# Kernel tuning notes

Hardware: AMD Instinct MI355X
Metric: run time of the kernel (lower is better)

The kernel has to match this reference:

```python
import jax, jax.numpy as jnp
import numpy as np

N = 65536   # nodes
E = 524288  # edges (avg degree 8)
IN, H, Z = 256, 128, 32
LN_EPS = 1e-5


def setup_inputs() -> dict:
    key = jax.random.key(0)
    ks = jax.random.split(key, 6)
    x = jax.random.normal(ks[0], (N, IN), jnp.float32)
    edge_index = jax.random.randint(ks[1], (2, E), 0, N, jnp.int32)
    W1 = jax.random.normal(ks[2], (IN, H), jnp.float32) / np.sqrt(IN)
    W2 = jax.random.normal(ks[3], (H, H), jnp.float32) / np.sqrt(H)
    W3 = jax.random.normal(ks[4], (H, Z), jnp.float32) / np.sqrt(H)
    return dict(
        x=x, edge_index=edge_index,
        ln_w=jnp.ones((IN,), jnp.float32), ln_b=jnp.zeros((IN,), jnp.float32),
        W1=W1, b1=jnp.zeros((H,), jnp.float32),
        W2=W2, b2=jnp.zeros((H,), jnp.float32),
        W3=W3, b3=jnp.zeros((Z,), jnp.float32),
    )


def _layer_norm(x, w, b):
    mu = jnp.mean(x, axis=-1, keepdims=True)
    var = jnp.mean(jnp.square(x - mu), axis=-1, keepdims=True)
    return (x - mu) * jax.lax.rsqrt(var + LN_EPS) * w + b


def _gcn_conv(x, W, b, src, dst, n):
    # PyG GCNConv: transform, add self-loops, symmetric deg normalization, scatter-add.
    x = x @ W  # [N, out]
    ones = jnp.ones(src.shape[0], x.dtype)
    deg = jax.ops.segment_sum(ones, dst, num_segments=n) + 1.0  # +1 self-loop
    dis = jax.lax.rsqrt(deg)  # deg^{-1/2}
    norm = dis[src] * dis[dst]  # [E]
    agg = jax.ops.segment_sum(x[src] * norm[:, None], dst, num_segments=n)
    agg = agg + x * (dis * dis)[:, None]  # self-loop term: dis[i]*dis[i]
    return agg + b


def reference(x, edge_index, ln_w, ln_b, W1, b1, W2, b2, W3, b3):
    src, dst = edge_index[0], edge_index[1]
    n = x.shape[0]
    h = _layer_norm(x, ln_w, ln_b)
    h = jax.nn.relu(_gcn_conv(h, W1, b1, src, dst, n))
    # dropout is identity in eval mode
    h = jax.nn.relu(_gcn_conv(h, W2, b2, src, dst, n))
    return _gcn_conv(h, W3, b3, src, dst, n)
```

## Files before the change

kernel.cpp:

```cpp
#include <hip/hip_runtime.h>
#include <hip/hip_bf16.h>

#define FIN 256
#define FH 128
#define FZ 32

typedef unsigned short u16;
typedef unsigned int u32;
typedef __attribute__((ext_vector_type(4))) float f32x4;
typedef __attribute__((ext_vector_type(8))) _Float16 f16x8;
typedef __attribute__((ext_vector_type(4))) _Float16 f16x4;
typedef __attribute__((ext_vector_type(4))) unsigned int uint4v;

__device__ inline u16 f2h(float v) { return __builtin_bit_cast(u16, (_Float16)v); }

__global__ __launch_bounds__(256) void prep(const float* __restrict__ W1,
                                            const float* __restrict__ W2,
                                            const float* __restrict__ W3,
                                            u16* __restrict__ w1h, u16* __restrict__ w2h,
                                            u16* __restrict__ w3h, int* __restrict__ deg,
                                            int* __restrict__ total) {
    int b = blockIdx.x, t = threadIdx.x;
    if (b < 256) {
        deg[b * 256 + t] = 0;
        if (b == 0 && t == 0) *total = 0;
        return;
    }
    int i = (b - 256) * 256 + t;
    if (i < FIN * FH) {
        int k = i / FH, n = i % FH;
        w1h[n * FIN + k] = f2h(W1[i]);
    } else if (i < FIN * FH + FH * FH) {
        int j = i - FIN * FH;
        int k = j / FH, n = j % FH;
        w2h[n * FH + k] = f2h(W2[j]);
    } else {
        int j = i - (FIN * FH + FH * FH);
        int k = j / FZ, n = j % FZ;
        w3h[n * FH + k] = f2h(W3[j]);
    }
}

__global__ void deg_count(const int* __restrict__ dst, int* __restrict__ deg,
                          int* __restrict__ erank, int E) {
    int e = blockIdx.x * 256 + threadIdx.x;
    if (e < E) erank[e] = atomicAdd(&deg[dst[e]], 1);
}

__global__ __launch_bounds__(256) void scan_fused(const int* __restrict__ deg,
                                                  int* __restrict__ total,
                                                  int* __restrict__ rowstart,
                                                  float* __restrict__ dis) {
    __shared__ int s[256];
    __shared__ int base;
    int t = threadIdx.x;
    int i = blockIdx.x * 256 + t;
    int v = deg[i];
    s[t] = v;
    __syncthreads();
    for (int o = 1; o < 256; o <<= 1) {
        int add = (t >= o) ? s[t - o] : 0;
        __syncthreads();
        s[t] += add;
        __syncthreads();
    }
    if (t == 255) base = atomicAdd(total, s[255]);
    __syncthreads();
    rowstart[i] = s[t] - v + base;
    dis[i] = rsqrtf((float)v + 1.0f);
}

__global__ __launch_bounds__(512) void gemm_ln(
    const float* __restrict__ Xf, const u16* __restrict__ Wg,
    const float* __restrict__ lnw, const float* __restrict__ lnb,
    const float* __restrict__ dis, u16* __restrict__ Y,
    const int* __restrict__ src, const int* __restrict__ dst,
    const int* __restrict__ erank, const int* __restrict__ rowstart,
    int* __restrict__ csrc, int E) {
    constexpr int K = FIN, N = FH;
    constexpr int BM = 128, NT = N / 16, NK = K / 32;

    __shared__ u16 Wl[N * K];

    const int t = threadIdx.x;
    const int row0 = blockIdx.x * BM;
    const int wave = t >> 6, l = t & 63;
    const int lm = l & 15, lq = l >> 4;
    const int row = row0 + wave * 16 + lm;

    const float* xr = Xf + (long long)row * K;
    f16x8 a[NK];
    float s = 0.f, ss = 0.f;
#pragma unroll
    for (int kk = 0; kk < NK; ++kk) {
        f32x4 x0 = *(const f32x4*)(xr + kk * 32 + lq * 8);
        f32x4 x1 = *(const f32x4*)(xr + kk * 32 + lq * 8 + 4);
#pragma unroll
        for (int c = 0; c < 4; ++c) {
            s += x0[c] + x1[c];
            ss += x0[c] * x0[c] + x1[c] * x1[c];
            a[kk][c] = (_Float16)x0[c];
            a[kk][4 + c] = (_Float16)x1[c];
        }
    }
    s += __shfl_xor(s, 16);
    ss += __shfl_xor(ss, 16);
    s += __shfl_xor(s, 32);
    ss += __shfl_xor(ss, 32);
    float mu = s * (1.0f / K);
    float rs = rsqrtf(fmaxf(ss * (1.0f / K) - mu * mu, 0.f) + 1e-5f);

    for (int i = t; i < N * K / 8; i += 512) {
        int nn = i / (K / 8), k8 = i % (K / 8);
        *(uint4v*)&Wl[nn * K + ((k8 ^ (nn & 7)) * 8)] = *(const uint4v*)&Wg[nn * K + k8 * 8];
    }

#pragma unroll
    for (int kk = 0; kk < NK; ++kk) {
        f32x4 w0 = *(const f32x4*)(lnw + kk * 32 + lq * 8);
        f32x4 w1 = *(const f32x4*)(lnw + kk * 32 + lq * 8 + 4);
        f32x4 c0 = *(const f32x4*)(lnb + kk * 32 + lq * 8);
        f32x4 c1 = *(const f32x4*)(lnb + kk * 32 + lq * 8 + 4);
#pragma unroll
        for (int c = 0; c < 4; ++c) {
            a[kk][c] = (_Float16)(((float)a[kk][c] - mu) * rs * w0[c] + c0[c]);
            a[kk][4 + c] = (_Float16)(((float)a[kk][4 + c] - mu) * rs * w1[c] + c1[c]);
        }
    }
    __syncthreads();

    f32x4 acc[NT];
#pragma unroll
    for (int i = 0; i < NT; ++i) acc[i] = (f32x4){0.f, 0.f, 0.f, 0.f};
#pragma unroll
    for (int kk = 0; kk < NK; ++kk) {
#pragma unroll
        for (int nt = 0; nt < NT; ++nt) {
            int nn = nt * 16 + lm;
            f16x8 wv = *(const f16x8*)&Wl[nn * K + (((kk * 4 + lq) ^ (nn & 7)) * 8)];
            acc[nt] = __builtin_amdgcn_mfma_f32_16x16x32_f16(wv, a[kk], acc[nt], 0, 0, 0);
        }
    }

    const float di = dis[row];
    u16* yr = Y + (long long)row * N;
#pragma unroll
    for (int nt = 0; nt < NT; ++nt) {
        f16x4 v;
#pragma unroll
        for (int r = 0; r < 4; ++r) v[r] = (_Float16)(acc[nt][r] * di);
        *(f16x4*)&yr[nt * 16 + lq * 4] = v;
    }

    {
        int epb = E / gridDim.x;
        int base = blockIdx.x * epb;
        for (int j = t; j < epb; j += 512) {
            int e = base + j;
            int d = dst[e];
            csrc[rowstart[d] + erank[e]] = src[e];
        }
    }
}

template <int K, int N>
__global__ __launch_bounds__(512) void gather_gemm(
    const u16* __restrict__ T, const u16* __restrict__ Wg,
    const int* __restrict__ rowstart, const int* __restrict__ degv,
    const int* __restrict__ csrc, const float* __restrict__ dis,
    const float* __restrict__ bias, u16* __restrict__ Y) {
    constexpr int BM = 128, NT = N / 16, NK = K / 32;

    __shared__ u16 Wl[N * K];
    __shared__ float bl[K];

    const int t = threadIdx.x;
    const int row0 = blockIdx.x * BM;
    const int wave = t >> 6, l = t & 63;
    const int lm = l & 15, lq = l >> 4;
    const int row = row0 + wave * 16 + lm;

    for (int i = t; i < N * K / 8; i += 512) {
        int nn = i / (K / 8), k8 = i % (K / 8);
        *(uint4v*)&Wl[nn * K + ((k8 ^ (nn & 7)) * 8)] = *(const uint4v*)&Wg[nn * K + k8 * 8];
    }
    if (t < K / 4) *(f32x4*)&bl[t * 4] = *(const f32x4*)&bias[t * 4];

    const float di = dis[row];
    const int rs = rowstart[row], dg = degv[row];
    float g[NK][8];
    {
        const u16* tr = T + (long long)row * K;
#pragma unroll
        for (int kk = 0; kk < NK; ++kk) {
            f16x8 v = *(const f16x8*)&tr[kk * 32 + lq * 8];
#pragma unroll
            for (int j = 0; j < 8; ++j) g[kk][j] = (float)v[j];
        }
    }
    int e = rs, e1 = rs + dg;
    for (; e + 1 < e1; e += 2) {
        int s0 = csrc[e], s1 = csrc[e + 1];
        const u16* t0 = T + (long long)s0 * K;
        const u16* t1 = T + (long long)s1 * K;
#pragma unroll
        for (int kk = 0; kk < NK; ++kk) {
            f16x8 v0 = *(const f16x8*)&t0[kk * 32 + lq * 8];
            f16x8 v1 = *(const f16x8*)&t1[kk * 32 + lq * 8];
#pragma unroll
            for (int j = 0; j < 8; ++j) g[kk][j] += (float)v0[j] + (float)v1[j];
        }
    }
    if (e < e1) {
        const u16* t0 = T + (long long)csrc[e] * K;
#pragma unroll
        for (int kk = 0; kk < NK; ++kk) {
            f16x8 v0 = *(const f16x8*)&t0[kk * 32 + lq * 8];
#pragma unroll
            for (int j = 0; j < 8; ++j) g[kk][j] += (float)v0[j];
        }
    }
    __syncthreads();

    f16x8 a[NK];
#pragma unroll
    for (int kk = 0; kk < NK; ++kk) {
#pragma unroll
        for (int j = 0; j < 8; ++j) {
            float h = fmaxf(g[kk][j] * di + bl[kk * 32 + lq * 8 + j], 0.f);
            a[kk][j] = (_Float16)h;
        }
    }

    f32x4 acc[NT];
#pragma unroll
    for (int i = 0; i < NT; ++i) acc[i] = (f32x4){0.f, 0.f, 0.f, 0.f};
#pragma unroll
    for (int kk = 0; kk < NK; ++kk) {
#pragma unroll
        for (int nt = 0; nt < NT; ++nt) {
            int nn = nt * 16 + lm;
            f16x8 wv = *(const f16x8*)&Wl[nn * K + (((kk * 4 + lq) ^ (nn & 7)) * 8)];
            acc[nt] = __builtin_amdgcn_mfma_f32_16x16x32_f16(wv, a[kk], acc[nt], 0, 0, 0);
        }
    }

    u16* yr = Y + (long long)row * N;
#pragma unroll
    for (int nt = 0; nt < NT; ++nt) {
        f16x4 v;
#pragma unroll
        for (int r = 0; r < 4; ++r) v[r] = (_Float16)(acc[nt][r] * di);
        *(f16x4*)&yr[nt * 16 + lq * 4] = v;
    }
}

__global__ __launch_bounds__(256) void agg32h(
    const u16* __restrict__ T, const int* __restrict__ rowstart, const int* __restrict__ degv,
    const int* __restrict__ csrc, const float* __restrict__ dis, const float* __restrict__ bias,
    float* __restrict__ OUT) {
    int node = blockIdx.x * 4 + (threadIdx.x >> 6);
    int l = threadIdx.x & 63;
    int h = l >> 3, c = l & 7;
    float di = dis[node];
    f32x4 acc = (f32x4){0.f, 0.f, 0.f, 0.f};
    if (h == 0) {
        f16x4 s = *(const f16x4*)&T[(long long)node * 32 + c * 4];
#pragma unroll
        for (int i = 0; i < 4; ++i) acc[i] = (float)s[i];
    }
    int e0 = rowstart[node];
    int e1 = e0 + degv[node];
    int e = e0 + h;
    for (; e + 8 < e1; e += 16) {
        int s0 = csrc[e], s1 = csrc[e + 8];
        f16x4 u0 = *(const f16x4*)&T[(long long)s0 * 32 + c * 4];
        f16x4 u1 = *(const f16x4*)&T[(long long)s1 * 32 + c * 4];
#pragma unroll
        for (int i = 0; i < 4; ++i) acc[i] += (float)u0[i] + (float)u1[i];
    }
    if (e < e1) {
        int s0 = csrc[e];
        f16x4 u0 = *(const f16x4*)&T[(long long)s0 * 32 + c * 4];
#pragma unroll
        for (int i = 0; i < 4; ++i) acc[i] += (float)u0[i];
    }
#pragma unroll
    for (int m = 8; m <= 32; m <<= 1) {
#pragma unroll
        for (int i = 0; i < 4; ++i) acc[i] += __shfl_xor(acc[i], m);
    }
    if (h == 0) {
        f32x4 b0 = *(const f32x4*)(bias + c * 4);
        f32x4 r;
#pragma unroll
        for (int i = 0; i < 4; ++i) r[i] = acc[i] * di + b0[i];
        *(f32x4*)(OUT + (long long)node * 32 + c * 4) = r;
    }
}

extern "C" void kernel_launch(void* const* d_in, const int* in_sizes, int n_in,
                              void* d_out, int out_size, void* d_ws, size_t ws_size,
                              hipStream_t stream) {
    const float* x = (const float*)d_in[0];
    const int* ei = (const int*)d_in[1];
    const float* lnw = (const float*)d_in[2];
    const float* lnb = (const float*)d_in[3];
    const float* W1 = (const float*)d_in[4];
    const float* b1 = (const float*)d_in[5];
    const float* W2 = (const float*)d_in[6];
    const float* b2 = (const float*)d_in[7];
    const float* W3 = (const float*)d_in[8];
    const float* b3 = (const float*)d_in[9];
    float* out = (float*)d_out;

    const int n = in_sizes[0] / FIN;
    const int E = in_sizes[1] / 2;
    const int* src = ei;
    const int* dst = ei + E;

    char* w = (char*)d_ws;
    auto alloc = [&](size_t bytes) {
        char* p = w;
        w += (bytes + 255) & ~(size_t)255;
        return p;
    };
    int* deg = (int*)alloc((size_t)n * 4);
    int* rowstart = (int*)alloc((size_t)n * 4);
    int* erank = (int*)alloc((size_t)E * 4);
    int* total = (int*)alloc(256);
    float* dis = (float*)alloc((size_t)n * 4);
    int* csrc = (int*)alloc((size_t)E * 4);
    u16* w1h = (u16*)alloc(FIN * FH * 2);
    u16* w2h = (u16*)alloc(FH * FH * 2);
    u16* w3h = (u16*)alloc(FH * FZ * 2);
    u16* bufA = (u16*)alloc((size_t)n * FH * 2);
    u16* bufB = (u16*)alloc((size_t)n * FH * 2);

    prep<<<464, 256, 0, stream>>>(W1, W2, W3, w1h, w2h, w3h, deg, total);
    deg_count<<<E / 256, 256, 0, stream>>>(dst, deg, erank, E);
    scan_fused<<<n / 256, 256, 0, stream>>>(deg, total, rowstart, dis);
    gemm_ln<<<n / 128, 512, 0, stream>>>(x, w1h, lnw, lnb, dis, bufA,
                                         src, dst, erank, rowstart, csrc, E);
    gather_gemm<FH, FH><<<n / 128, 512, 0, stream>>>(bufA, w2h, rowstart, deg, csrc, dis, b1, bufB);
    gather_gemm<FH, FZ><<<n / 128, 512, 0, stream>>>(bufB, w3h, rowstart, deg, csrc, dis, b2, bufA);
    agg32h<<<n / 4, 256, 0, stream>>>(bufA, rowstart, deg, csrc, dis, b3, out);
}
```

Measured before the change: 145.1 us.

## Fuse weight prep with degree count, double rows per gemm_ln block, unroll gather

```diff
diff --git a/kernel.cpp b/kernel.cpp
--- a/kernel.cpp
+++ b/kernel.cpp
@@ -14,19 +14,17 @@
 
 __device__ inline u16 f2h(float v) { return __builtin_bit_cast(u16, (_Float16)v); }
 
-__global__ __launch_bounds__(256) void prep(const float* __restrict__ W1,
-                                            const float* __restrict__ W2,
-                                            const float* __restrict__ W3,
-                                            u16* __restrict__ w1h, u16* __restrict__ w2h,
-                                            u16* __restrict__ w3h, int* __restrict__ deg,
-                                            int* __restrict__ total) {
+__global__ __launch_bounds__(256) void prep_deg(
+    const float* __restrict__ W1, const float* __restrict__ W2, const float* __restrict__ W3,
+    u16* __restrict__ w1h, u16* __restrict__ w2h, u16* __restrict__ w3h,
+    const int* __restrict__ dst, int* __restrict__ deg, int* __restrict__ erank, int E) {
     int b = blockIdx.x, t = threadIdx.x;
-    if (b < 256) {
-        deg[b * 256 + t] = 0;
-        if (b == 0 && t == 0) *total = 0;
+    if (b >= 208) {
+        int e = (b - 208) * 256 + t;
+        if (e < E) erank[e] = atomicAdd(&deg[dst[e]], 1);
         return;
     }
-    int i = (b - 256) * 256 + t;
+    int i = b * 256 + t;
     if (i < FIN * FH) {
         int k = i / FH, n = i % FH;
         w1h[n * FIN + k] = f2h(W1[i]);
@@ -39,12 +37,6 @@
         int k = j / FZ, n = j % FZ;
         w3h[n * FH + k] = f2h(W3[j]);
     }
-}
-
-__global__ void deg_count(const int* __restrict__ dst, int* __restrict__ deg,
-                          int* __restrict__ erank, int E) {
-    int e = blockIdx.x * 256 + threadIdx.x;
-    if (e < E) erank[e] = atomicAdd(&deg[dst[e]], 1);
 }
 
 __global__ __launch_bounds__(256) void scan_fused(const int* __restrict__ deg,
@@ -70,7 +62,7 @@
     dis[i] = rsqrtf((float)v + 1.0f);
 }
 
-__global__ __launch_bounds__(512) void gemm_ln(
+__global__ __launch_bounds__(512, 4) void gemm_ln(
     const float* __restrict__ Xf, const u16* __restrict__ Wg,
     const float* __restrict__ lnw, const float* __restrict__ lnb,
     const float* __restrict__ dis, u16* __restrict__ Y,
@@ -78,43 +70,43 @@
     const int* __restrict__ erank, const int* __restrict__ rowstart,
     int* __restrict__ csrc, int E) {
     constexpr int K = FIN, N = FH;
-    constexpr int BM = 128, NT = N / 16, NK = K / 32;
+    constexpr int NT = N / 16, NK = K / 32;
 
     __shared__ u16 Wl[N * K];
 
     const int t = threadIdx.x;
-    const int row0 = blockIdx.x * BM;
     const int wave = t >> 6, l = t & 63;
     const int lm = l & 15, lq = l >> 4;
-    const int row = row0 + wave * 16 + lm;
-
-    const float* xr = Xf + (long long)row * K;
-    f16x8 a[NK];
-    float s = 0.f, ss = 0.f;
-#pragma unroll
-    for (int kk = 0; kk < NK; ++kk) {
-        f32x4 x0 = *(const f32x4*)(xr + kk * 32 + lq * 8);
-        f32x4 x1 = *(const f32x4*)(xr + kk * 32 + lq * 8 + 4);
+    const int row0 = blockIdx.x * 256 + wave * 16 + lm;
+    const int row1 = row0 + 128;
+
+    const float* xr0 = Xf + (long long)row0 * K;
+    f16x8 a0[NK];
+    float s0 = 0.f, ss0 = 0.f;
+#pragma unroll
+    for (int kk = 0; kk < NK; ++kk) {
+        f32x4 x0 = *(const f32x4*)(xr0 + kk * 32 + lq * 8);
+        f32x4 x1 = *(const f32x4*)(xr0 + kk * 32 + lq * 8 + 4);
 #pragma unroll
         for (int c = 0; c < 4; ++c) {
-            s += x0[c] + x1[c];
-            ss += x0[c] * x0[c] + x1[c] * x1[c];
-            a[kk][c] = (_Float16)x0[c];
-            a[kk][4 + c] = (_Float16)x1[c];
-        }
-    }
-    s += __shfl_xor(s, 16);
-    ss += __shfl_xor(ss, 16);
-    s += __shfl_xor(s, 32);
-    ss += __shfl_xor(ss, 32);
-    float mu = s * (1.0f / K);
-    float rs = rsqrtf(fmaxf(ss * (1.0f / K) - mu * mu, 0.f) + 1e-5f);
+            s0 += x0[c] + x1[c];
+            ss0 += x0[c] * x0[c] + x1[c] * x1[c];
+            a0[kk][c] = (_Float16)x0[c];
+            a0[kk][4 + c] = (_Float16)x1[c];
+        }
+    }
 
     for (int i = t; i < N * K / 8; i += 512) {
         int nn = i / (K / 8), k8 = i % (K / 8);
         *(uint4v*)&Wl[nn * K + ((k8 ^ (nn & 7)) * 8)] = *(const uint4v*)&Wg[nn * K + k8 * 8];
     }
 
+    s0 += __shfl_xor(s0, 16);
+    ss0 += __shfl_xor(ss0, 16);
+    s0 += __shfl_xor(s0, 32);
+    ss0 += __shfl_xor(ss0, 32);
+    float mu0 = s0 * (1.0f / K);
+    float rs0 = rsqrtf(fmaxf(ss0 * (1.0f / K) - mu0 * mu0, 0.f) + 1e-5f);
 #pragma unroll
     for (int kk = 0; kk < NK; ++kk) {
         f32x4 w0 = *(const f32x4*)(lnw + kk * 32 + lq * 8);
@@ -123,11 +115,27 @@
         f32x4 c1 = *(const f32x4*)(lnb + kk * 32 + lq * 8 + 4);
 #pragma unroll
         for (int c = 0; c < 4; ++c) {
-            a[kk][c] = (_Float16)(((float)a[kk][c] - mu) * rs * w0[c] + c0[c]);
-            a[kk][4 + c] = (_Float16)(((float)a[kk][4 + c] - mu) * rs * w1[c] + c1[c]);
+            a0[kk][c] = (_Float16)(((float)a0[kk][c] - mu0) * rs0 * w0[c] + c0[c]);
+            a0[kk][4 + c] = (_Float16)(((float)a0[kk][4 + c] - mu0) * rs0 * w1[c] + c1[c]);
         }
     }
     __syncthreads();
+
+    const float* xr1 = Xf + (long long)row1 * K;
+    f16x8 a1[NK];
+    float s1 = 0.f, ss1 = 0.f;
+#pragma unroll
+    for (int kk = 0; kk < NK; ++kk) {
+        f32x4 x0 = *(const f32x4*)(xr1 + kk * 32 + lq * 8);
+        f32x4 x1 = *(const f32x4*)(xr1 + kk * 32 + lq * 8 + 4);
+#pragma unroll
+        for (int c = 0; c < 4; ++c) {
+            s1 += x0[c] + x1[c];
+            ss1 += x0[c] * x0[c] + x1[c] * x1[c];
+            a1[kk][c] = (_Float16)x0[c];
+            a1[kk][4 + c] = (_Float16)x1[c];
+        }
+    }
 
     f32x4 acc[NT];
 #pragma unroll
@@ -138,18 +146,61 @@
         for (int nt = 0; nt < NT; ++nt) {
             int nn = nt * 16 + lm;
             f16x8 wv = *(const f16x8*)&Wl[nn * K + (((kk * 4 + lq) ^ (nn & 7)) * 8)];
-            acc[nt] = __builtin_amdgcn_mfma_f32_16x16x32_f16(wv, a[kk], acc[nt], 0, 0, 0);
-        }
-    }
-
-    const float di = dis[row];
-    u16* yr = Y + (long long)row * N;
-#pragma unroll
-    for (int nt = 0; nt < NT; ++nt) {
-        f16x4 v;
-#pragma unroll
-        for (int r = 0; r < 4; ++r) v[r] = (_Float16)(acc[nt][r] * di);
-        *(f16x4*)&yr[nt * 16 + lq * 4] = v;
+            acc[nt] = __builtin_amdgcn_mfma_f32_16x16x32_f16(wv, a0[kk], acc[nt], 0, 0, 0);
+        }
+    }
+    {
+        const float di = dis[row0];
+        u16* yr = Y + (long long)row0 * N;
+#pragma unroll
+        for (int nt = 0; nt < NT; ++nt) {
+            f16x4 v;
+#pragma unroll
+            for (int r = 0; r < 4; ++r) v[r] = (_Float16)(acc[nt][r] * di);
+            *(f16x4*)&yr[nt * 16 + lq * 4] = v;
+        }
+    }
+
+    s1 += __shfl_xor(s1, 16);
+    ss1 += __shfl_xor(ss1, 16);
+    s1 += __shfl_xor(s1, 32);
+    ss1 += __shfl_xor(ss1, 32);
+    float mu1 = s1 * (1.0f / K);
+    float rs1 = rsqrtf(fmaxf(ss1 * (1.0f / K) - mu1 * mu1, 0.f) + 1e-5f);
+#pragma unroll
+    for (int kk = 0; kk < NK; ++kk) {
+        f32x4 w0 = *(const f32x4*)(lnw + kk * 32 + lq * 8);
+        f32x4 w1 = *(const f32x4*)(lnw + kk * 32 + lq * 8 + 4);
+        f32x4 c0 = *(const f32x4*)(lnb + kk * 32 + lq * 8);
+        f32x4 c1 = *(const f32x4*)(lnb + kk * 32 + lq * 8 + 4);
+#pragma unroll
+        for (int c = 0; c < 4; ++c) {
+            a1[kk][c] = (_Float16)(((float)a1[kk][c] - mu1) * rs1 * w0[c] + c0[c]);
+            a1[kk][4 + c] = (_Float16)(((float)a1[kk][4 + c] - mu1) * rs1 * w1[c] + c1[c]);
+        }
+    }
+
+#pragma unroll
+    for (int i = 0; i < NT; ++i) acc[i] = (f32x4){0.f, 0.f, 0.f, 0.f};
+#pragma unroll
+    for (int kk = 0; kk < NK; ++kk) {
+#pragma unroll
+        for (int nt = 0; nt < NT; ++nt) {
+            int nn = nt * 16 + lm;
+            f16x8 wv = *(const f16x8*)&Wl[nn * K + (((kk * 4 + lq) ^ (nn & 7)) * 8)];
+            acc[nt] = __builtin_amdgcn_mfma_f32_16x16x32_f16(wv, a1[kk], acc[nt], 0, 0, 0);
+        }
+    }
+    {
+        const float di = dis[row1];
+        u16* yr = Y + (long long)row1 * N;
+#pragma unroll
+        for (int nt = 0; nt < NT; ++nt) {
+            f16x4 v;
+#pragma unroll
+            for (int r = 0; r < 4; ++r) v[r] = (_Float16)(acc[nt][r] * di);
+            *(f16x4*)&yr[nt * 16 + lq * 4] = v;
+        }
     }
 
     {
@@ -199,19 +250,24 @@
         }
     }
     int e = rs, e1 = rs + dg;
-    for (; e + 1 < e1; e += 2) {
-        int s0 = csrc[e], s1 = csrc[e + 1];
-        const u16* t0 = T + (long long)s0 * K;
-        const u16* t1 = T + (long long)s1 * K;
+    for (; e + 3 < e1; e += 4) {
+        int i0 = csrc[e], i1 = csrc[e + 1], i2 = csrc[e + 2], i3 = csrc[e + 3];
+        const u16* t0 = T + (long long)i0 * K;
+        const u16* t1 = T + (long long)i1 * K;
+        const u16* t2 = T + (long long)i2 * K;
+        const u16* t3 = T + (long long)i3 * K;
 #pragma unroll
         for (int kk = 0; kk < NK; ++kk) {
             f16x8 v0 = *(const f16x8*)&t0[kk * 32 + lq * 8];
             f16x8 v1 = *(const f16x8*)&t1[kk * 32 + lq * 8];
-#pragma unroll
-            for (int j = 0; j < 8; ++j) g[kk][j] += (float)v0[j] + (float)v1[j];
-        }
-    }
-    if (e < e1) {
+            f16x8 v2 = *(const f16x8*)&t2[kk * 32 + lq * 8];
+            f16x8 v3 = *(const f16x8*)&t3[kk * 32 + lq * 8];
+#pragma unroll
+            for (int j = 0; j < 8; ++j)
+                g[kk][j] += ((float)v0[j] + (float)v1[j]) + ((float)v2[j] + (float)v3[j]);
+        }
+    }
+    for (; e < e1; ++e) {
         const u16* t0 = T + (long long)csrc[e] * K;
 #pragma unroll
         for (int kk = 0; kk < NK; ++kk) {
@@ -326,9 +382,9 @@
         return p;
     };
     int* deg = (int*)alloc((size_t)n * 4);
+    int* total = (int*)alloc(256);
     int* rowstart = (int*)alloc((size_t)n * 4);
     int* erank = (int*)alloc((size_t)E * 4);
-    int* total = (int*)alloc(256);
     float* dis = (float*)alloc((size_t)n * 4);
     int* csrc = (int*)alloc((size_t)E * 4);
     u16* w1h = (u16*)alloc(FIN * FH * 2);
@@ -337,10 +393,10 @@
     u16* bufA = (u16*)alloc((size_t)n * FH * 2);
     u16* bufB = (u16*)alloc((size_t)n * FH * 2);
 
-    prep<<<464, 256, 0, stream>>>(W1, W2, W3, w1h, w2h, w3h, deg, total);
-    deg_count<<<E / 256, 256, 0, stream>>>(dst, deg, erank, E);
+    hipMemsetAsync(deg, 0, (size_t)n * 4 + 256, stream);
+    prep_deg<<<208 + E / 256, 256, 0, stream>>>(W1, W2, W3, w1h, w2h, w3h, dst, deg, erank, E);
     scan_fused<<<n / 256, 256, 0, stream>>>(deg, total, rowstart, dis);
-    gemm_ln<<<n / 128, 512, 0, stream>>>(x, w1h, lnw, lnb, dis, bufA,
+    gemm_ln<<<n / 256, 512, 0, stream>>>(x, w1h, lnw, lnb, dis, bufA,
                                          src, dst, erank, rowstart, csrc, E);
     gather_gemm<FH, FH><<<n / 128, 512, 0, stream>>>(bufA, w2h, rowstart, deg, csrc, dis, b1, bufB);
     gather_gemm<FH, FZ><<<n / 128, 512, 0, stream>>>(bufB, w3h, rowstart, deg, csrc, dis, b2, bufA);
```

Result: slower. 168.0 us (+15.8%).
